# Performance work log

Hardware: AMD Instinct MI355X
Metric: run time of the kernel (lower is better)

Reference implementation:

```python
import jax, jax.numpy as jnp
import numpy as np

STRIDES = [1, 2, 4, 8]
K = 512  # num_nodes_per_scale
HID = 128
OUT = 128


def conv1x1(x, w, b):
    # x: [B,C,H,W], w: [O,C], b: [O]
    return jnp.einsum('bchw,oc->bohw', x, w) + b[None, :, None, None]


def head(x, w1, b1, w2, b2):
    # Conv1x1 -> exact GELU -> Conv1x1 (matches nn.GELU default)
    return conv1x1(jax.nn.gelu(conv1x1(x, w1, b1), approximate=False), w2, b2)


def max_pool(x, r):
    # torch max_pool2d(kernel=2r+1, stride=1, padding=r) pads with -inf
    k = 2 * r + 1
    return jax.lax.reduce_window(x, -jnp.inf, jax.lax.max,
                                 (1, 1, k, k), (1, 1, 1, 1),
                                 [(0, 0), (0, 0), (r, r), (r, r)])


def simple_nms(w, r):
    ninf = jnp.asarray(-jnp.inf, w.dtype)
    max_mask = w == max_pool(w, r)
    for _ in range(2):
        supp_mask = max_pool(max_mask.astype(w.dtype), r) > 0
        supp_w = jnp.where(supp_mask, ninf, w)
        new_max = supp_w == max_pool(supp_w, r)
        max_mask = max_mask | (new_max & ~supp_mask)
    return jnp.where(max_mask, w, ninf)


def bilinear_sample(feat, gx, gy):
    # grid_sample(mode='bilinear', align_corners=False, padding_mode='zeros')
    # feat: [B,C,H,W]; gx,gy: [B,K] normalized coords in [-1,1]
    B, C, H, W = feat.shape
    ix = ((gx + 1.0) * W - 1.0) * 0.5
    iy = ((gy + 1.0) * H - 1.0) * 0.5
    x0 = jnp.floor(ix); y0 = jnp.floor(iy)
    x1 = x0 + 1.0;      y1 = y0 + 1.0
    wx1 = ix - x0;      wy1 = iy - y0
    flat = feat.reshape(B, C, H * W)

    def gather(xc, yc):
        valid = (xc >= 0) & (xc <= W - 1) & (yc >= 0) & (yc <= H - 1)
        xi = jnp.clip(xc, 0, W - 1).astype(jnp.int32)
        yi = jnp.clip(yc, 0, H - 1).astype(jnp.int32)
        lin = yi * W + xi  # [B,K]
        g = jnp.take_along_axis(flat, lin[:, None, :], axis=2)  # [B,C,K]
        return g * valid[:, None, :].astype(feat.dtype)

    v00 = gather(x0, y0); v01 = gather(x1, y0)
    v10 = gather(x0, y1); v11 = gather(x1, y1)
    out = (v00 * ((1 - wx1) * (1 - wy1))[:, None, :]
           + v01 * (wx1 * (1 - wy1))[:, None, :]
           + v10 * ((1 - wx1) * wy1)[:, None, :]
           + v11 * (wx1 * wy1)[:, None, :])
    return out.transpose(0, 2, 1)  # [B,K,C]


def process_scale(fm, rw1, rb1, rw2, rb2, fw1, fb1, fw2, fb2):
    B, C, H, W = fm.shape
    rel = head(fm, rw1, rb1, rw2, rb2)   # [B,1,H,W]
    proj = head(fm, fw1, fb1, fw2, fb2)  # [B,OUT,H,W]
    border = max(1, H // 64)
    r = max(1, H // 64)
    m = jnp.zeros((H, W), bool).at[border:H - border, border:W - border].set(True)
    rel = jnp.where(m[None, None], rel, -jnp.inf)
    rel = simple_nms(rel, r)
    vals, idx = jax.lax.top_k(rel.reshape(B, H * W), K)  # [B,K]
    y = idx // W
    x = idx % W
    nx = x.astype(jnp.float32) / (W - 1) * 2.0 - 1.0
    ny = y.astype(jnp.float32) / (H - 1) * 2.0 - 1.0
    feats = bilinear_sample(proj, nx, ny)  # [B,K,OUT]
    return jnp.stack([nx, ny], axis=-1), vals, feats


def setup_inputs() -> dict:
    key = jax.random.key(0)
    ks = jax.random.split(key, 12)
    B = 2
    inp = {
        'fm1': jax.random.normal(ks[0], (B, HID, 512, 512), jnp.float32),
        'fm2': jax.random.normal(ks[1], (B, HID, 256, 256), jnp.float32),
        'fm4': jax.random.normal(ks[2], (B, HID, 128, 128), jnp.float32),
        'fm8': jax.random.normal(ks[3], (B, HID, 64, 64), jnp.float32),
        'rw1': jax.random.normal(ks[4], (OUT, HID), jnp.float32) * 0.05,
        'rb1': jnp.zeros((OUT,), jnp.float32),
        'rw2': jax.random.normal(ks[5], (1, OUT), jnp.float32) * 0.05,
        'rb2': jnp.zeros((1,), jnp.float32),
        'fw1': jax.random.normal(ks[6], (OUT, HID), jnp.float32) * 0.05,
        'fb1': jnp.zeros((OUT,), jnp.float32),
        'fw2': jax.random.normal(ks[7], (OUT, OUT), jnp.float32) * 0.05,
        'fb2': jnp.zeros((OUT,), jnp.float32),
    }
    return inp


def reference(fm1, fm2, fm4, fm8, rw1, rb1, rw2, rb2, fw1, fb1, fw2, fb2):
    outs = [process_scale(fm, rw1, rb1, rw2, rb2, fw1, fb1, fw2, fb2)
            for fm in (fm1, fm2, fm4, fm8)]
    all_norm_xy = jnp.concatenate([o[0] for o in outs], axis=1)      # [B,4K,2]
    all_reliability = jnp.concatenate([o[1] for o in outs], axis=1)  # [B,4K]
    all_features = jnp.concatenate([o[2] for o in outs], axis=1)     # [B,4K,OUT]
    return all_norm_xy, all_reliability, all_features
```

## Files before the change

kernel.cpp:

```cpp
#include <hip/hip_runtime.h>
#include <math.h>

#define CH 128
#define KSEL 512
#define CAP 4096
#define TOT 2048
#define TS 32
#define NEG_INF (-__builtin_inff())

typedef short s8v __attribute__((ext_vector_type(8)));
typedef float f4v __attribute__((ext_vector_type(4)));

__device__ __forceinline__ float gelu_exact(float v) {
    return v * 0.5f * (1.0f + erff(v * 0.70710678118654752440f));
}

__device__ __forceinline__ void split3(float v, unsigned short& h,
                                       unsigned short& m, unsigned short& l)
{
    union { float f; unsigned u; } a; a.f = v;
    unsigned rh = a.u + 0x7FFFu + ((a.u >> 16) & 1u);
    h = (unsigned short)(rh >> 16);
    union { unsigned u; float f; } fh; fh.u = rh & 0xFFFF0000u;
    float r1 = v - fh.f;
    union { float f; unsigned u; } bu; bu.f = r1;
    unsigned rm = bu.u + 0x7FFFu + ((bu.u >> 16) & 1u);
    m = (unsigned short)(rm >> 16);
    union { unsigned u; float f; } fm2; fm2.u = rm & 0xFFFF0000u;
    float r2 = r1 - fm2.f;
    union { float f; unsigned u; } cu; cu.f = r2;
    unsigned rl = cu.u + 0x7FFFu + ((cu.u >> 16) & 1u);
    l = (unsigned short)(rl >> 16);
}

__global__ __launch_bounds__(256) void wconv_kernel(const float* __restrict__ w1,
                                                    unsigned short* __restrict__ wfrag)
{
    for (int e = blockIdx.x * 256 + threadIdx.x; e < 49152; e += gridDim.x * 256) {
        int fid = e >> 9;
        int r = e & 511;
        int lane = r >> 3;
        int el = r & 7;
        int plane = fid % 3;
        int fq = fid / 3;
        int kc = fq >> 3, ot = fq & 7;
        int och = ot * 16 + (lane & 15);
        int k = kc * 32 + ((lane >> 4) << 3) + el;
        unsigned short h, m, l;
        split3(w1[och * CH + k], h, m, l);
        wfrag[e] = (plane == 0) ? h : (plane == 1) ? m : l;
    }
}

__global__ __launch_bounds__(512) void rel_mfma_kernel(
    const float* __restrict__ fm0, const float* __restrict__ fm1,
    const float* __restrict__ fm2, const float* __restrict__ fm3,
    const unsigned short* __restrict__ wfrag,
    const float* __restrict__ b1, const float* __restrict__ w2,
    const float* __restrict__ b2, float* __restrict__ rel)
{
    __shared__ uint4 WfQ[6144];
    __shared__ float w2s[128], b1s[128];
    unsigned short* Wf = (unsigned short*)WfQ;

    const int tid = threadIdx.x;
    {
        const uint4* src = (const uint4*)wfrag;
        for (int i = tid; i < 6144; i += 512) WfQ[i] = src[i];
    }
    if (tid < 128) { w2s[tid] = w2[tid]; b1s[tid] = b1[tid]; }
    __syncthreads();

    const float* fms[4] = {fm0, fm1, fm2, fm3};
    const int pre1 = 2048, pre2 = 2560, pre3 = 2688;
    const int relo[4] = {0, 524288, 655360, 688128};
    const float b2v = b2[0];

    const int lane = tid & 63;
    const int j = lane & 15;
    const int g8 = (lane >> 4) << 3;
    const int w = tid >> 6;

    for (int T = blockIdx.x; T < 2720; T += gridDim.x) {
        int s = (T >= pre1) + (T >= pre2) + (T >= pre3);
        int t2 = T - ((s == 0) ? 0 : (s == 1) ? pre1 : (s == 2) ? pre2 : pre3);
        int Wd = 512 >> s, HW = Wd * Wd;
        int p0 = t2 * 256 + w * 32;
        int b = (p0 >= HW) ? 1 : 0;
        int pb = p0 - b * HW;
        const float* fp = fms[s] + (size_t)b * CH * HW;
        int rr = Wd >> 6; if (rr < 1) rr = 1;

        const float* pxp = fp + pb + 2 * j;

        f4v acc[8][2];
        #pragma unroll
        for (int ot = 0; ot < 8; ++ot)
            #pragma unroll
            for (int st = 0; st < 2; ++st) {
                acc[ot][st][0] = 0.f; acc[ot][st][1] = 0.f;
                acc[ot][st][2] = 0.f; acc[ot][st][3] = 0.f;
            }

        #pragma unroll 1
        for (int kc = 0; kc < 4; ++kc) {
            float2 xv[8];
            #pragma unroll
            for (int e = 0; e < 8; ++e)
                xv[e] = *(const float2*)(pxp + (size_t)(kc * 32 + g8 + e) * HW);

            s8v bh0, bm0, bl0, bh1, bm1, bl1;
            #pragma unroll
            for (int e = 0; e < 8; ++e) {
                unsigned short h, m, l;
                split3(xv[e].x, h, m, l);
                bh0[e] = (short)h; bm0[e] = (short)m; bl0[e] = (short)l;
                split3(xv[e].y, h, m, l);
                bh1[e] = (short)h; bm1[e] = (short)m; bl1[e] = (short)l;
            }
            #pragma unroll
            for (int ot = 0; ot < 8; ++ot) {
                const unsigned short* fb = Wf + (((kc << 3) + ot) * 3) * 512 + (lane << 3);
                s8v ah = *(const s8v*)fb;
                s8v am = *(const s8v*)(fb + 512);
                s8v al = *(const s8v*)(fb + 1024);
                acc[ot][0] = __builtin_amdgcn_mfma_f32_16x16x32_bf16(ah, bh0, acc[ot][0], 0, 0, 0);
                acc[ot][0] = __builtin_amdgcn_mfma_f32_16x16x32_bf16(ah, bm0, acc[ot][0], 0, 0, 0);
                acc[ot][0] = __builtin_amdgcn_mfma_f32_16x16x32_bf16(am, bh0, acc[ot][0], 0, 0, 0);
                acc[ot][0] = __builtin_amdgcn_mfma_f32_16x16x32_bf16(am, bm0, acc[ot][0], 0, 0, 0);
                acc[ot][0] = __builtin_amdgcn_mfma_f32_16x16x32_bf16(ah, bl0, acc[ot][0], 0, 0, 0);
                acc[ot][0] = __builtin_amdgcn_mfma_f32_16x16x32_bf16(al, bh0, acc[ot][0], 0, 0, 0);
                acc[ot][1] = __builtin_amdgcn_mfma_f32_16x16x32_bf16(ah, bh1, acc[ot][1], 0, 0, 0);
                acc[ot][1] = __builtin_amdgcn_mfma_f32_16x16x32_bf16(ah, bm1, acc[ot][1], 0, 0, 0);
                acc[ot][1] = __builtin_amdgcn_mfma_f32_16x16x32_bf16(am, bh1, acc[ot][1], 0, 0, 0);
                acc[ot][1] = __builtin_amdgcn_mfma_f32_16x16x32_bf16(am, bm1, acc[ot][1], 0, 0, 0);
                acc[ot][1] = __builtin_amdgcn_mfma_f32_16x16x32_bf16(ah, bl1, acc[ot][1], 0, 0, 0);
                acc[ot][1] = __builtin_amdgcn_mfma_f32_16x16x32_bf16(al, bh1, acc[ot][1], 0, 0, 0);
            }
        }

        float part0 = 0.f, part1 = 0.f;
        #pragma unroll
        for (int ot = 0; ot < 8; ++ot) {
            #pragma unroll
            for (int r = 0; r < 4; ++r) {
                int och = ot * 16 + ((lane >> 4) << 2) + r;
                float wv = w2s[och], bv = b1s[och];
                part0 += wv * gelu_exact(acc[ot][0][r] + bv);
                part1 += wv * gelu_exact(acc[ot][1][r] + bv);
            }
        }
        part0 += __shfl_xor(part0, 16);
        part0 += __shfl_xor(part0, 32);
        part1 += __shfl_xor(part1, 16);
        part1 += __shfl_xor(part1, 32);
        if (lane < 16) {
            int p0x = pb + 2 * lane;
            int y0 = p0x / Wd, x0 = p0x - y0 * Wd;
            int p1x = p0x + 1;
            int y1 = p1x / Wd, x1 = p1x - y1 * Wd;
            bool in0 = (y0 >= rr) && (y0 < Wd - rr) && (x0 >= rr) && (x0 < Wd - rr);
            bool in1 = (y1 >= rr) && (y1 < Wd - rr) && (x1 >= rr) && (x1 < Wd - rr);
            float2 o;
            o.x = in0 ? (part0 + b2v) : NEG_INF;
            o.y = in1 ? (part1 + b2v) : NEG_INF;
            *(float2*)&rel[relo[s] + b * HW + p0x] = o;
        }
    }
}

__device__ __forceinline__ void nms_decode(int blk, int& s, int& b, int& ty, int& tx,
                                           int& Wd, int& HW, int& r, int& ro)
{
    s = (blk >= 512) + (blk >= 640) + (blk >= 672);
    int t2 = blk - ((s == 0) ? 0 : (s == 1) ? 512 : (s == 2) ? 640 : 672);
    Wd = 512 >> s; HW = Wd * Wd;
    int tpb = (Wd / TS) * (Wd / TS);
    b = t2 / tpb;
    int t = t2 - b * tpb;
    ty = t / (Wd / TS); tx = t - ty * (Wd / TS);
    r = Wd >> 6; if (r < 1) r = 1;
    ro = (s == 0) ? 0 : (s == 1) ? 524288 : (s == 2) ? 655360 : 688128;
}

__global__ __launch_bounds__(256) void nms_init_all(
    const float* __restrict__ rel, float* __restrict__ mask)
{
    int s, b, ty, tx, W, HW, r, ro;
    nms_decode(blockIdx.x, s, b, ty, tx, W, HW, r, ro);
    int H = W;
    int L = TS + 2 * r;
    __shared__ float wtile[48][49];
    __shared__ float t1[48][49];
    const float* wp = rel + ro + (size_t)b * HW;
    for (int idx = threadIdx.x; idx < L * L; idx += 256) {
        int i = idx / L, j = idx - i * L;
        int gy = min(max(ty * TS - r + i, 0), H - 1);
        int gx = min(max(tx * TS - r + j, 0), W - 1);
        wtile[i][j] = wp[gy * W + gx];
    }
    __syncthreads();
    for (int idx = threadIdx.x; idx < L * TS; idx += 256) {
        int i = idx / TS, j = idx - i * TS;
        float m = wtile[i][j];
        for (int d = 1; d <= 2 * r; ++d) m = fmaxf(m, wtile[i][j + d]);
        t1[i][j] = m;
    }
    __syncthreads();
    for (int idx = threadIdx.x; idx < TS * TS; idx += 256) {
        int i = idx / TS, j = idx - i * TS;
        float m = t1[i][j];
        for (int d = 1; d <= 2 * r; ++d) m = fmaxf(m, t1[i + d][j]);
        mask[ro + (size_t)b * HW + (ty * TS + i) * W + (tx * TS + j)] =
            (wtile[i + r][j + r] == m) ? 1.0f : 0.0f;
    }
}

__global__ __launch_bounds__(256) void nms_fused_all(
    const float* __restrict__ rel, float* __restrict__ mask, int do_compact,
    float* __restrict__ lval, int* __restrict__ lidx, int* __restrict__ counts)
{
    int s, b, ty, tx, W, HW, r, ro;
    nms_decode(blockIdx.x, s, b, ty, tx, W, HW, r, ro);
    int H = W;
    int L = TS + 4 * r;
    int gy0 = ty * TS - 2 * r, gx0 = tx * TS - 2 * r;
    __shared__ float A[64][65], B[64][65], C[64][65];
    const float* mp = mask + ro + (size_t)b * HW;
    const float* rp = rel + ro + (size_t)b * HW;

    for (int idx = threadIdx.x; idx < L * L; idx += 256) {
        int i = idx / L, j = idx - i * L;
        int gy = min(max(gy0 + i, 0), H - 1);
        int gx = min(max(gx0 + j, 0), W - 1);
        A[i][j] = mp[gy * W + gx];
    }
    __syncthreads();
    int w1c = L - 2 * r;
    for (int idx = threadIdx.x; idx < L * w1c; idx += 256) {
        int i = idx / w1c, j = idx - i * w1c + r;
        float m = A[i][j - r];
        for (int d = 1; d <= 2 * r; ++d) m = fmaxf(m, A[i][j - r + d]);
        B[i][j] = m;
    }
    __syncthreads();
    for (int idx = threadIdx.x; idx < w1c * w1c; idx += 256) {
        int i = idx / w1c + r, j = idx % w1c + r;
        float m = B[i - r][j];
        for (int d = 1; d <= 2 * r; ++d) m = fmaxf(m, B[i - r + d][j]);
        C[i][j] = m;
    }
    float mreg[4];
    #pragma unroll
    for (int k = 0; k < 4; ++k) {
        int idx = threadIdx.x + k * 256;
        int i = idx >> 5, j = idx & 31;
        mreg[k] = A[2 * r + i][2 * r + j];
    }
    __syncthreads();
    for (int idx = threadIdx.x; idx < w1c * w1c; idx += 256) {
        int i = idx / w1c + r, j = idx % w1c + r;
        int gy = min(max(gy0 + i, 0), H - 1);
        int gx = min(max(gx0 + j, 0), W - 1);
        B[i][j] = (C[i][j] > 0.f) ? NEG_INF : rp[gy * W + gx];
    }
    __syncthreads();
    for (int idx = threadIdx.x; idx < w1c * TS; idx += 256) {
        int i = idx / TS + r, j = idx % TS + 2 * r;
        float m = B[i][j - r];
        for (int d = 1; d <= 2 * r; ++d) m = fmaxf(m, B[i][j - r + d]);
        A[i][j] = m;
    }
    __syncthreads();
    #pragma unroll
    for (int k = 0; k < 4; ++k) {
        int idx = threadIdx.x + k * 256;
        int i = idx >> 5, j = idx & 31;
        int ci = 2 * r + i, cj = 2 * r + j;
        float m = A[ci - r][cj];
        for (int d = 1; d <= 2 * r; ++d) m = fmaxf(m, A[ci - r + d][cj]);
        bool supp = C[ci][cj] > 0.f;
        bool newm = (B[ci][cj] == m) && !supp;
        bool fin = (mreg[k] > 0.f) || newm;
        int gy = ty * TS + i, gx = tx * TS + j;
        size_t g = ro + (size_t)b * HW + gy * W + gx;
        if (!do_compact) {
            mask[g] = fin ? 1.f : 0.f;
        } else if (fin) {
            float v = rp[gy * W + gx];
            if (!isinf(v)) {
                int bs = b * 4 + s;
                int slot = atomicAdd(&counts[bs], 1);
                if (slot < CAP) { lval[bs * CAP + slot] = v; lidx[bs * CAP + slot] = gy * W + gx; }
            }
        }
    }
}

__global__ __launch_bounds__(1024) void sort_topk_kernel(
    const float* __restrict__ lval, const int* __restrict__ lidx,
    const int* __restrict__ counts, float* __restrict__ tv, int* __restrict__ ti)
{
    __shared__ float sv[CAP];
    __shared__ int   si[CAP];
    int bs = blockIdx.x;
    int M = counts[bs]; if (M > CAP) M = CAP;
    for (int i = threadIdx.x; i < CAP; i += 1024) {
        if (i < M) { sv[i] = lval[bs * CAP + i]; si[i] = lidx[bs * CAP + i]; }
        else       { sv[i] = NEG_INF;            si[i] = 0x7FFFFFFF; }
    }
    __syncthreads();
    for (int k = 2; k <= CAP; k <<= 1) {
        for (int j = k >> 1; j > 0; j >>= 1) {
            for (int t = threadIdx.x; t < CAP; t += 1024) {
                int p = t ^ j;
                if (p > t) {
                    float va = sv[t], vb = sv[p];
                    int   ia = si[t], ib = si[p];
                    bool aBefore = (va > vb) || (va == vb && ia < ib);
                    bool up = ((t & k) == 0);
                    if (up ? !aBefore : aBefore) {
                        sv[t] = vb; sv[p] = va; si[t] = ib; si[p] = ia;
                    }
                }
            }
            __syncthreads();
        }
    }
    for (int j = threadIdx.x; j < KSEL; j += 1024) {
        if (j < M) { tv[bs * KSEL + j] = sv[j]; ti[bs * KSEL + j] = si[j]; }
        else       { tv[bs * KSEL + j] = NEG_INF; ti[bs * KSEL + j] = j - M; }
    }
}

__global__ __launch_bounds__(256) void coords_kernel(
    const float* __restrict__ tv, const int* __restrict__ ti, float* __restrict__ out)
{
    int gid = blockIdx.x * blockDim.x + threadIdx.x;
    if (gid >= 8 * KSEL) return;
    int bs = gid / KSEL, k = gid - bs * KSEL;
    int b = bs >> 2, s = bs & 3;
    int W = 512 >> s;
    int idx = ti[gid];
    int y = idx / W, x = idx - y * W;
    float nx = (float)x / (float)(W - 1) * 2.0f - 1.0f;
    float ny = (float)y / (float)(W - 1) * 2.0f - 1.0f;
    int pos = s * KSEL + k;
    out[((size_t)b * TOT + pos) * 2 + 0] = nx;
    out[((size_t)b * TOT + pos) * 2 + 1] = ny;
    out[2 * TOT * 2 + (size_t)b * TOT + pos] = tv[gid];
}

__global__ __launch_bounds__(128) void feats_kernel(
    const float* __restrict__ fm0, const float* __restrict__ fm1,
    const float* __restrict__ fm2, const float* __restrict__ fm3,
    const float* __restrict__ w1, const float* __restrict__ b1,
    const float* __restrict__ w2, const float* __restrict__ b2,
    const int* __restrict__ ti, float* __restrict__ out)
{
    int blk = blockIdx.x;
    int bs = blk / KSEL, k = blk - bs * KSEL;
    int b = bs >> 2, s = bs & 3;
    int W = 512 >> s, H = W, HW = H * W;
    const float* fm = (s == 0) ? fm0 : (s == 1) ? fm1 : (s == 2) ? fm2 : fm3;

    int idx = ti[bs * KSEL + k];
    int yi0 = idx / W, xi0 = idx - yi0 * W;
    float nx = (float)xi0 / (float)(W - 1) * 2.0f - 1.0f;
    float ny = (float)yi0 / (float)(H - 1) * 2.0f - 1.0f;
    float ix = ((nx + 1.0f) * (float)W - 1.0f) * 0.5f;
    float iy = ((ny + 1.0f) * (float)H - 1.0f) * 0.5f;
    float x0 = floorf(ix), y0 = floorf(iy);
    float x1 = x0 + 1.0f,  y1 = y0 + 1.0f;
    float wx1 = ix - x0, wy1 = iy - y0;

    float xs[4]  = {x0, x1, x0, x1};
    float ysv[4] = {y0, y0, y1, y1};
    float wn[4]  = {(1.0f - wx1) * (1.0f - wy1), wx1 * (1.0f - wy1),
                    (1.0f - wx1) * wy1,          wx1 * wy1};
    int pix[4]; float wv[4];
    #pragma unroll
    for (int n = 0; n < 4; ++n) {
        bool valid = (xs[n] >= 0.0f) && (xs[n] <= (float)(W - 1)) &&
                     (ysv[n] >= 0.0f) && (ysv[n] <= (float)(H - 1));
        int xc = (int)fminf(fmaxf(xs[n], 0.0f), (float)(W - 1));
        int yc = (int)fminf(fmaxf(ysv[n], 0.0f), (float)(H - 1));
        pix[n] = yc * W + xc;
        wv[n] = valid ? wn[n] : 0.0f;
    }

    __shared__ float xls[4][CH];
    __shared__ float hmix[CH];
    int o = threadIdx.x;
    {
        const float* fb_ = fm + ((size_t)b * CH + o) * HW;
        #pragma unroll
        for (int n = 0; n < 4; ++n) xls[n][o] = fb_[pix[n]];
    }
    __syncthreads();

    float h0 = b1[o], h1 = h0, h2 = h0, h3 = h0;
    const float* wr = w1 + o * CH;
    for (int c = 0; c < CH; ++c) {
        float w = wr[c];
        h0 = fmaf(w, xls[0][c], h0);
        h1 = fmaf(w, xls[1][c], h1);
        h2 = fmaf(w, xls[2][c], h2);
        h3 = fmaf(w, xls[3][c], h3);
    }
    float wsum = wv[0] + wv[1] + wv[2] + wv[3];
    hmix[o] = wv[0] * gelu_exact(h0) + wv[1] * gelu_exact(h1) +
              wv[2] * gelu_exact(h2) + wv[3] * gelu_exact(h3);
    __syncthreads();

    float acc = b2[o] * wsum;
    const float* w2r = w2 + o * CH;
    for (int c = 0; c < CH; ++c) acc = fmaf(w2r[c], hmix[c], acc);
    out[2 * TOT * 2 + 2 * TOT + ((size_t)b * TOT + s * KSEL + k) * CH + o] = acc;
}

extern "C" void kernel_launch(void* const* d_in, const int* in_sizes, int n_in,
                              void* d_out, int out_size, void* d_ws, size_t ws_size,
                              hipStream_t stream)
{
    const float* fm[4] = {(const float*)d_in[0], (const float*)d_in[1],
                          (const float*)d_in[2], (const float*)d_in[3]};
    const float* rw1 = (const float*)d_in[4];
    const float* rb1 = (const float*)d_in[5];
    const float* rw2 = (const float*)d_in[6];
    const float* rb2 = (const float*)d_in[7];
    const float* fw1 = (const float*)d_in[8];
    const float* fb1 = (const float*)d_in[9];
    const float* fw2 = (const float*)d_in[10];
    const float* fb2 = (const float*)d_in[11];

    float* ws = (float*)d_ws;
    float* rel   = ws;
    float* mask  = ws + 696320;
    float* lval  = ws + 1392640;
    int*   lidx  = (int*)(ws + 1425408);
    int*   counts= (int*)(ws + 1458176);
    float* tv    = ws + 1458184;
    int*   ti    = (int*)(ws + 1462280);
    unsigned short* wfrag = (unsigned short*)(ws + 1466376);

    hipMemsetAsync(counts, 0, 8 * sizeof(int), stream);
    wconv_kernel<<<64, 256, 0, stream>>>(rw1, wfrag);
    rel_mfma_kernel<<<256, 512, 0, stream>>>(fm[0], fm[1], fm[2], fm[3],
                                             wfrag, rb1, rw2, rb2, rel);

    nms_init_all<<<680, 256, 0, stream>>>(rel, mask);
    nms_fused_all<<<680, 256, 0, stream>>>(rel, mask, 0, lval, lidx, counts);
    nms_fused_all<<<680, 256, 0, stream>>>(rel, mask, 1, lval, lidx, counts);

    sort_topk_kernel<<<8, 1024, 0, stream>>>(lval, lidx, counts, tv, ti);
    coords_kernel<<<16, 256, 0, stream>>>(tv, ti, (float*)d_out);
    feats_kernel<<<4096, 128, 0, stream>>>(fm[0], fm[1], fm[2], fm[3],
                                           fw1, fb1, fw2, fb2, ti, (float*)d_out);
}
```

Before: 498.8 us.

## Merge NMS init and first suppression pass into one halo-tiled kernel

Replaces the separate max-mask init kernel and the first NMS suppression pass with a single kernel. It loads a larger tile of the reliability map (halo 3r) into shared memory and computes the initial max mask, its dilation, the suppressed scores and the updated mask all on-chip. This removes one kernel launch and a global round trip of the mask buffer. In exchange it recomputes halo regions per tile, needs much more shared memory (four 80x81 float arrays), and has more barriers, which can lower occupancy.

```diff
diff --git a/kernel.cpp b/kernel.cpp
--- a/kernel.cpp
+++ b/kernel.cpp
@@ -183,36 +183,84 @@
     ro = (s == 0) ? 0 : (s == 1) ? 524288 : (s == 2) ? 655360 : 688128;
 }
 
-__global__ __launch_bounds__(256) void nms_init_all(
+__global__ __launch_bounds__(256) void nms_merged_all(
     const float* __restrict__ rel, float* __restrict__ mask)
 {
     int s, b, ty, tx, W, HW, r, ro;
     nms_decode(blockIdx.x, s, b, ty, tx, W, HW, r, ro);
     int H = W;
-    int L = TS + 2 * r;
-    __shared__ float wtile[48][49];
-    __shared__ float t1[48][49];
-    const float* wp = rel + ro + (size_t)b * HW;
+    int L = TS + 6 * r;
+    int g0y = ty * TS - 3 * r, g0x = tx * TS - 3 * r;
+    __shared__ float R[80][81], A[80][81], B[80][81], C[80][81];
+    const float* rp = rel + ro + (size_t)b * HW;
+
     for (int idx = threadIdx.x; idx < L * L; idx += 256) {
         int i = idx / L, j = idx - i * L;
-        int gy = min(max(ty * TS - r + i, 0), H - 1);
-        int gx = min(max(tx * TS - r + j, 0), W - 1);
-        wtile[i][j] = wp[gy * W + gx];
-    }
-    __syncthreads();
-    for (int idx = threadIdx.x; idx < L * TS; idx += 256) {
-        int i = idx / TS, j = idx - i * TS;
-        float m = wtile[i][j];
-        for (int d = 1; d <= 2 * r; ++d) m = fmaxf(m, wtile[i][j + d]);
-        t1[i][j] = m;
-    }
-    __syncthreads();
-    for (int idx = threadIdx.x; idx < TS * TS; idx += 256) {
-        int i = idx / TS, j = idx - i * TS;
-        float m = t1[i][j];
-        for (int d = 1; d <= 2 * r; ++d) m = fmaxf(m, t1[i + d][j]);
-        mask[ro + (size_t)b * HW + (ty * TS + i) * W + (tx * TS + j)] =
-            (wtile[i + r][j + r] == m) ? 1.0f : 0.0f;
+        int gy = min(max(g0y + i, 0), H - 1);
+        int gx = min(max(g0x + j, 0), W - 1);
+        R[i][j] = rp[gy * W + gx];
+    }
+    __syncthreads();
+    int w1 = L - 2 * r;
+    for (int idx = threadIdx.x; idx < L * w1; idx += 256) {
+        int i = idx / w1, j = idx % w1 + r;
+        float m = R[i][j - r];
+        for (int d = 1; d <= 2 * r; ++d) m = fmaxf(m, R[i][j - r + d]);
+        C[i][j] = m;
+    }
+    __syncthreads();
+    for (int idx = threadIdx.x; idx < w1 * w1; idx += 256) {
+        int i = idx / w1 + r, j = idx % w1 + r;
+        float m = C[i - r][j];
+        for (int d = 1; d <= 2 * r; ++d) m = fmaxf(m, C[i - r + d][j]);
+        A[i][j] = (R[i][j] == m) ? 1.f : 0.f;
+    }
+    __syncthreads();
+    int w2 = L - 4 * r;
+    for (int idx = threadIdx.x; idx < w1 * w2; idx += 256) {
+        int i = idx / w2 + r, j = idx % w2 + 2 * r;
+        float m = A[i][j - r];
+        for (int d = 1; d <= 2 * r; ++d) m = fmaxf(m, A[i][j - r + d]);
+        B[i][j] = m;
+    }
+    __syncthreads();
+    for (int idx = threadIdx.x; idx < w2 * w2; idx += 256) {
+        int i = idx / w2 + 2 * r, j = idx % w2 + 2 * r;
+        float m = B[i - r][j];
+        for (int d = 1; d <= 2 * r; ++d) m = fmaxf(m, B[i - r + d][j]);
+        C[i][j] = m;
+    }
+    float mreg[4];
+    #pragma unroll
+    for (int k = 0; k < 4; ++k) {
+        int idx = threadIdx.x + k * 256;
+        int i = idx >> 5, j = idx & 31;
+        mreg[k] = A[3 * r + i][3 * r + j];
+    }
+    __syncthreads();
+    for (int idx = threadIdx.x; idx < w2 * w2; idx += 256) {
+        int i = idx / w2 + 2 * r, j = idx % w2 + 2 * r;
+        B[i][j] = (C[i][j] > 0.f) ? NEG_INF : R[i][j];
+    }
+    __syncthreads();
+    for (int idx = threadIdx.x; idx < w2 * TS; idx += 256) {
+        int i = idx / TS + 2 * r, j = idx % TS + 3 * r;
+        float m = B[i][j - r];
+        for (int d = 1; d <= 2 * r; ++d) m = fmaxf(m, B[i][j - r + d]);
+        A[i][j] = m;
+    }
+    __syncthreads();
+    #pragma unroll
+    for (int k = 0; k < 4; ++k) {
+        int idx = threadIdx.x + k * 256;
+        int i = idx >> 5, j = idx & 31;
+        int ci = 3 * r + i, cj = 3 * r + j;
+        float m = A[ci - r][cj];
+        for (int d = 1; d <= 2 * r; ++d) m = fmaxf(m, A[ci - r + d][cj]);
+        bool supp = C[ci][cj] > 0.f;
+        bool newm = (B[ci][cj] == m) && !supp;
+        bool fin = (mreg[k] > 0.f) || newm;
+        mask[ro + (size_t)b * HW + (ty * TS + i) * W + (tx * TS + j)] = fin ? 1.f : 0.f;
     }
 }
 
@@ -449,8 +497,7 @@
     rel_mfma_kernel<<<256, 512, 0, stream>>>(fm[0], fm[1], fm[2], fm[3],
                                              wfrag, rb1, rw2, rb2, rel);
 
-    nms_init_all<<<680, 256, 0, stream>>>(rel, mask);
-    nms_fused_all<<<680, 256, 0, stream>>>(rel, mask, 0, lval, lidx, counts);
+    nms_merged_all<<<680, 256, 0, stream>>>(rel, mask);
     nms_fused_all<<<680, 256, 0, stream>>>(rel, mask, 1, lval, lidx, counts);
 
     sort_topk_kernel<<<8, 1024, 0, stream>>>(lval, lidx, counts, tv, ti);
```

New measurement: 604.5 us. 1.21x slower.
